# Kernel optimization log

Measured on AMD Instinct MI355X. Metric: run time of the kernel, lower is better.

## Reference

```python
import jax, jax.numpy as jnp
import numpy as np

N = 30000      # points
E = 400000     # edges
CIN = 16       # input point features
B = 4          # graphs in batch
H, W = 60, 80  # BEV grid


def _mlp_params(key, cin, cout):
    k1, k2 = jax.random.split(key)
    wa = jax.random.normal(k1, (cin, cout), jnp.float32) * np.float32(np.sqrt(2.0 / cin))
    wb = jax.random.normal(k2, (cout, cout), jnp.float32) * np.float32(np.sqrt(2.0 / cout))
    return wa, jnp.zeros((cout,), jnp.float32), wb, jnp.zeros((cout,), jnp.float32)


def setup_inputs() -> dict:
    key = jax.random.key(0)
    ks = jax.random.split(key, 8)
    x = jax.random.normal(ks[0], (N, CIN), jnp.float32)
    r = jax.random.uniform(ks[1], (N, 3), jnp.float32)
    Z = 1.0 + 9.0 * r[:, 2]
    X = (r[:, 0] - 0.5) * 1.2 * Z   # |X/Z| < 0.6 -> mostly inside image
    Y = (r[:, 1] - 0.5) * 0.9 * Z
    pos = jnp.stack([X, Y, Z], axis=1)
    edge_index = jax.random.randint(ks[2], (2, E), 0, N, jnp.int32)
    batch = jnp.sort(jax.random.randint(ks[3], (N,), 0, B, jnp.int32))
    K = jnp.array([[500.0, 0.0, 320.0], [0.0, 500.0, 240.0], [0.0, 0.0, 1.0]], jnp.float32)
    w11, b11, w12, b12 = _mlp_params(ks[4], CIN + 3, 64)
    w21, b21, w22, b22 = _mlp_params(ks[5], 64 + 3, 128)
    w31, b31, w32, b32 = _mlp_params(ks[6], 128 + 3, 256)
    return dict(x=x, pos=pos, K=K,
                w11=w11, b11=b11, w12=w12, b12=b12,
                w21=w21, b21=b21, w22=w22, b22=b22,
                w31=w31, b31=b31, w32=w32, b32=b32,
                edge_index=edge_index, batch=batch)


def _mlp(h, wa, ba, wb, bb):
    return jax.nn.relu(h @ wa + ba) @ wb + bb


def _pointnet_conv(feat, rel, src, dst, wa, ba, wb, bb):
    # PyG PointNetConv: msg = local_nn([x_j, pos_j - pos_i]); max-aggregate at target i
    msg = _mlp(jnp.concatenate([feat[src], rel], axis=1), wa, ba, wb, bb)
    agg = jax.ops.segment_max(msg, dst, num_segments=N)
    return jnp.where(jnp.isfinite(agg), agg, 0.0)  # empty segments -> 0 (PyG fill)


def _points_to_image(feat, pos, batch, K):
    X, Y, Z = pos[:, 0], pos[:, 1], pos[:, 2]
    u = ((K[0, 0] * X / Z + K[0, 2]) / 640.0 * W).astype(jnp.int32)  # trunc like .long()
    v = ((K[1, 1] * Y / Z + K[1, 2]) / 480.0 * H).astype(jnp.int32)
    mask = (u >= 0) & (u < W) & (v >= 0) & (v < H)
    idx = jnp.where(mask, batch * (H * W) + v * W + u, 0)
    contrib = feat * mask[:, None].astype(feat.dtype)
    flat = jnp.zeros((B * H * W, feat.shape[1]), feat.dtype).at[idx].add(contrib)
    return flat.reshape(B, H, W, feat.shape[1]).transpose(0, 3, 1, 2)


def reference(x, pos, K, w11, b11, w12, b12, w21, b21, w22, b22, w31, b31, w32, b32,
              edge_index, batch):
    src, dst = edge_index[0], edge_index[1]
    rel = pos[src] - pos[dst]
    h = _pointnet_conv(x, rel, src, dst, w11, b11, w12, b12)
    h = _pointnet_conv(h, rel, src, dst, w21, b21, w22, b22)
    h = _pointnet_conv(h, rel, src, dst, w31, b31, w32, b32)
    return _points_to_image(h, pos, batch, K)  # [B, 256, H, W]
```

## Files before the change

kernel.cpp:

```cpp
#include <hip/hip_runtime.h>
#include <math.h>

#define NN 30000
#define NE 400000

typedef _Float16 f16;
typedef _Float16 f16x8 __attribute__((ext_vector_type(8)));
typedef float f32x4 __attribute__((ext_vector_type(4)));

__device__ __forceinline__ void atomic_max_f(float* addr, float v) {
    if (v >= 0.0f) {
        atomicMax((int*)addr, __float_as_int(v));
    } else {
        atomicMin((unsigned int*)addr, __float_as_uint(v));
    }
}

__global__ __launch_bounds__(256) void fill_neg_inf(float* p, int n) {
    int i = blockIdx.x * blockDim.x + threadIdx.x;
    int stride = gridDim.x * blockDim.x;
    for (; i < n; i += stride) p[i] = -INFINITY;
}

__global__ __launch_bounds__(256) void hist_dst(const int* __restrict__ dst,
                                                int* __restrict__ counts) {
    int e = blockIdx.x * 256 + threadIdx.x;
    if (e < NE) atomicAdd(&counts[dst[e]], 1);
}

__global__ __launch_bounds__(1024) void scan_counts(const int* __restrict__ counts,
                                                    int* __restrict__ cursor) {
    __shared__ int lsum[1024];
    const int t = threadIdx.x;
    const int base = t * 30;
    int s = 0;
    for (int i = 0; i < 30; ++i) {
        int idx = base + i;
        if (idx < NN) s += counts[idx];
    }
    lsum[t] = s;
    __syncthreads();
    int acc = s;
    for (int off = 1; off < 1024; off <<= 1) {
        int v = (t >= off) ? lsum[t - off] : 0;
        __syncthreads();
        acc += v;
        lsum[t] = acc;
        __syncthreads();
    }
    int run = acc - s;
    for (int i = 0; i < 30; ++i) {
        int idx = base + i;
        if (idx < NN) { cursor[idx] = run; run += counts[idx]; }
    }
}

__global__ __launch_bounds__(256) void scatter_edges(const int* __restrict__ src,
                                                     const int* __restrict__ dst,
                                                     int* __restrict__ cursor,
                                                     int* __restrict__ srcS,
                                                     int* __restrict__ dstS) {
    int e = blockIdx.x * 256 + threadIdx.x;
    if (e >= NE) return;
    int d = dst[e];
    int p = atomicAdd(&cursor[d], 1);
    srcS[p] = src[e];
    dstS[p] = d;
}

template<int K, int N>
__global__ __launch_bounds__(256) void pack_w(const float* __restrict__ wsrc,
                                              f16* __restrict__ pB) {
    int f = blockIdx.x * 256 + threadIdx.x;
    if (f >= K * N) return;
    int j = f & 7;
    int l = (f >> 3) & 63;
    int rest = f >> 9;
    constexpr int KS = K / 32;
    int ks = rest % KS;
    int nt = rest / KS;
    int k = ks * 32 + ((l >> 4) << 3) + j;
    int n = nt * 16 + (l & 15);
    pB[f] = (f16)wsrc[k * N + n];
}

template<int K, int COUT>
__global__ __launch_bounds__(256) void node_linear(const float* __restrict__ feat,
                                                   const float* __restrict__ wa,
                                                   const float* __restrict__ b,
                                                   f16* __restrict__ A) {
    constexpr int NPB = 8;
    constexpr int G   = 256 / COUT;
    constexpr int NPT = NPB / G;
    __shared__ float sf[NPB * K];
    const int node0 = blockIdx.x * NPB;
    for (int idx = threadIdx.x; idx < NPB * K; idx += 256) {
        float v = feat[node0 * K + idx];
        if (!isfinite(v)) v = 0.0f;
        sf[idx] = v;
    }
    __syncthreads();
    const int j  = threadIdx.x % COUT;
    const int g  = threadIdx.x / COUT;
    const int n0 = g * NPT;
    float acc[NPT];
#pragma unroll
    for (int i = 0; i < NPT; i++) acc[i] = 0.0f;
    for (int k = 0; k < K; k++) {
        float w = wa[k * COUT + j];
#pragma unroll
        for (int nn = 0; nn < NPT; nn++)
            acc[nn] = fmaf(sf[(n0 + nn) * K + k], w, acc[nn]);
    }
    const float bj = b[j];
#pragma unroll
    for (int nn = 0; nn < NPT; nn++)
        A[(size_t)(node0 + n0 + nn) * COUT + j] = (f16)(acc[nn] + bj);
}

template<int K, int C>
__global__ __launch_bounds__(256) void node_gemm(const float* __restrict__ feat,
                                                 const f16* __restrict__ pW,
                                                 const float* __restrict__ bias,
                                                 f16* __restrict__ A) {
    constexpr int NTW = C / 64;
    constexpr int KS  = K / 32;
    __shared__ __align__(16) unsigned char smem[64 * K * 2];
    const int tid = threadIdx.x;
    const int node0 = blockIdx.x * 64;

    {
        const int e = tid >> 2, p = tid & 3;
        const bool valid = (node0 + e) < NN;
        const float* frow = feat + (size_t)(node0 + e) * K;
#pragma unroll
        for (int ch = 0; ch < K / 32; ++ch) {
            const int j0 = (ch * 4 + p) * 8;
            f16x8 hv;
#pragma unroll
            for (int jj = 0; jj < 8; ++jj) {
                float v = valid ? frow[j0 + jj] : 0.0f;
                if (!isfinite(v)) v = 0.0f;
                hv[jj] = (f16)v;
            }
            *(f16x8*)(smem + e * (K * 2) + ((j0 * 2) ^ ((e & 7) << 4))) = hv;
        }
    }
    __syncthreads();

    const int w = tid >> 6, l = tid & 63, lr = l & 15, lg = l >> 4;
    f32x4 acc[4][NTW];
#pragma unroll
    for (int m = 0; m < 4; ++m)
#pragma unroll
        for (int nt = 0; nt < NTW; ++nt) {
            acc[m][nt][0] = 0.f; acc[m][nt][1] = 0.f;
            acc[m][nt][2] = 0.f; acc[m][nt][3] = 0.f;
        }
#pragma unroll
    for (int ks = 0; ks < KS; ++ks) {
        f16x8 af[4];
#pragma unroll
        for (int m = 0; m < 4; ++m) {
            const int row = m * 16 + lr;
            af[m] = *(const f16x8*)(smem + row * (K * 2)
                     + (((ks * 32 + lg * 8) * 2) ^ ((row & 7) << 4)));
        }
#pragma unroll
        for (int nt = 0; nt < NTW; ++nt) {
            const int ntg = w * NTW + nt;
            f16x8 bf = *(const f16x8*)(pW + ((size_t)(ntg * KS + ks) * 64 + l) * 8);
#pragma unroll
            for (int m = 0; m < 4; ++m)
                acc[m][nt] = __builtin_amdgcn_mfma_f32_16x16x32_f16(af[m], bf, acc[m][nt], 0, 0, 0);
        }
    }
#pragma unroll
    for (int m = 0; m < 4; ++m)
#pragma unroll
        for (int nt = 0; nt < NTW; ++nt) {
            const int col = w * (C / 4) + nt * 16 + lr;
            const float bv = bias[col];
#pragma unroll
            for (int rr = 0; rr < 4; ++rr) {
                const int row = m * 16 + lg * 4 + rr;
                if (node0 + row < NN)
                    A[(size_t)(node0 + row) * C + col] = (f16)(acc[m][nt][rr] + bv);
            }
        }
}

template<int C>
__global__ __launch_bounds__(256) void edge_mfma(const f16* __restrict__ Ah,
                                                 const float* __restrict__ warel,
                                                 const f16* __restrict__ pB,
                                                 const float* __restrict__ bb,
                                                 const float* __restrict__ pos,
                                                 const int* __restrict__ srcS,
                                                 const int* __restrict__ dstS,
                                                 float* __restrict__ agg) {
    constexpr int TE  = 64;
    constexpr int NTW = C / 64;
    constexpr int KS  = C / 32;
    __shared__ __align__(16) unsigned char smem[TE * C * 2];
    __shared__ float s_warel[3 * C];
    __shared__ float s_rx[TE], s_ry[TE], s_rz[TE];
    __shared__ int s_src[TE], s_dst[TE];

    const int tid = threadIdx.x;
    const int nwg = gridDim.x;
    const int q = nwg >> 3, r = nwg & 7;
    const int xcd = blockIdx.x & 7, o = blockIdx.x >> 3;
    const int bid = (xcd < r ? xcd * (q + 1) : r * (q + 1) + (xcd - r) * q) + o;
    const int e0 = bid * TE;

    if (tid < TE) {
        int s = srcS[e0 + tid], d = dstS[e0 + tid];
        s_src[tid] = s; s_dst[tid] = d;
        s_rx[tid] = pos[3 * s + 0] - pos[3 * d + 0];
        s_ry[tid] = pos[3 * s + 1] - pos[3 * d + 1];
        s_rz[tid] = pos[3 * s + 2] - pos[3 * d + 2];
    }
    for (int i = tid; i < 3 * C; i += 256) s_warel[i] = warel[i];
    __syncthreads();

    {
        const int e = tid >> 2, p = tid & 3;
        const int s = s_src[e];
        const float rx = s_rx[e], ry = s_ry[e], rz = s_rz[e];
        const f16* arow = Ah + (size_t)s * C;
#pragma unroll
        for (int ch = 0; ch < C / 32; ++ch) {
            const int j0 = (ch * 4 + p) * 8;
            f16x8 av = *(const f16x8*)(arow + j0);
            f16x8 hv;
#pragma unroll
            for (int jj = 0; jj < 8; ++jj) {
                int jc = j0 + jj;
                float v = (float)av[jj] + rx * s_warel[jc] + ry * s_warel[C + jc]
                        + rz * s_warel[2 * C + jc];
                hv[jj] = (f16)fmaxf(v, 0.0f);
            }
            *(f16x8*)(smem + e * (C * 2) + ((j0 * 2) ^ ((e & 7) << 4))) = hv;
        }
    }
    __syncthreads();

    const int w = tid >> 6, l = tid & 63, lr = l & 15, lg = l >> 4;
    f32x4 acc[4][NTW];
#pragma unroll
    for (int m = 0; m < 4; ++m)
#pragma unroll
        for (int nt = 0; nt < NTW; ++nt) {
            acc[m][nt][0] = 0.f; acc[m][nt][1] = 0.f;
            acc[m][nt][2] = 0.f; acc[m][nt][3] = 0.f;
        }
#pragma unroll
    for (int ks = 0; ks < KS; ++ks) {
        f16x8 af[4];
#pragma unroll
        for (int m = 0; m < 4; ++m) {
            const int row = m * 16 + lr;
            af[m] = *(const f16x8*)(smem + row * (C * 2)
                     + (((ks * 32 + lg * 8) * 2) ^ ((row & 7) << 4)));
        }
#pragma unroll
        for (int nt = 0; nt < NTW; ++nt) {
            const int ntg = w * NTW + nt;
            f16x8 bf = *(const f16x8*)(pB + ((size_t)(ntg * KS + ks) * 64 + l) * 8);
#pragma unroll
            for (int m = 0; m < 4; ++m)
                acc[m][nt] = __builtin_amdgcn_mfma_f32_16x16x32_f16(af[m], bf, acc[m][nt], 0, 0, 0);
        }
    }

    float* msg = (float*)smem;
    const int c = tid;
    const bool active = (c < C);
    const float bbv = active ? bb[c] : 0.0f;
    float run = -INFINITY;
    int prev = s_dst[0];
#pragma unroll
    for (int half = 0; half < 2; ++half) {
        __syncthreads();
#pragma unroll
        for (int mi = 0; mi < 2; ++mi) {
            const int m = half * 2 + mi;
#pragma unroll
            for (int nt = 0; nt < NTW; ++nt) {
                const int col = w * (C / 4) + nt * 16 + lr;
#pragma unroll
                for (int rr = 0; rr < 4; ++rr) {
                    const int row = m * 16 + lg * 4 + rr;
                    msg[(row - half * 32) * C + col] = acc[m][nt][rr];
                }
            }
        }
        __syncthreads();
        if (active) {
            for (int e2 = 0; e2 < 32; ++e2) {
                const int d = s_dst[half * 32 + e2];
                const float v = msg[e2 * C + c];
                if (d != prev) {
                    atomic_max_f(&agg[(size_t)prev * C + c], run + bbv);
                    run = v; prev = d;
                } else {
                    run = fmaxf(run, v);
                }
            }
        }
    }
    if (active) atomic_max_f(&agg[(size_t)prev * C + c], run + bbv);
}

__global__ __launch_bounds__(256) void scatter_img(const float* __restrict__ feat,
                                                   const float* __restrict__ pos,
                                                   const float* __restrict__ Km,
                                                   const int* __restrict__ batch,
                                                   float* __restrict__ img) {
    const int n = blockIdx.x;
    const float X = pos[3 * n + 0], Y = pos[3 * n + 1], Z = pos[3 * n + 2];
    const float k00 = Km[0], k02 = Km[2], k11 = Km[4], k12 = Km[5];
    const int u = (int)((k00 * X / Z + k02) / 640.0f * 80.0f);
    const int v = (int)((k11 * Y / Z + k12) / 480.0f * 60.0f);
    if (u < 0 || u >= 80 || v < 0 || v >= 60) return;
    const int p = (batch[n] * 60 + v) * 80 + u;
    const int c = threadIdx.x;
    float val = feat[(size_t)n * 256 + c];
    if (!isfinite(val)) val = 0.0f;
    atomicAdd(img + (size_t)p * 256 + c, val);
}

__global__ __launch_bounds__(256) void transpose_img(const float* __restrict__ img,
                                                     float* __restrict__ out) {
    __shared__ float tile[32][33];
    const int b = blockIdx.z;
    const int p0 = blockIdx.x * 32, c0 = blockIdx.y * 32;
    const float* src = img + (size_t)b * 4800 * 256;
    float* dst = out + (size_t)b * 256 * 4800;
    const int tx = threadIdx.x & 31, ty = threadIdx.x >> 5;
#pragma unroll
    for (int i = 0; i < 32; i += 8)
        tile[ty + i][tx] = src[(size_t)(p0 + ty + i) * 256 + c0 + tx];
    __syncthreads();
#pragma unroll
    for (int i = 0; i < 32; i += 8)
        dst[(size_t)(c0 + ty + i) * 4800 + p0 + tx] = tile[tx][ty + i];
}

extern "C" void kernel_launch(void* const* d_in, const int* in_sizes, int n_in,
                              void* d_out, int out_size, void* d_ws, size_t ws_size,
                              hipStream_t stream) {
    const float* x   = (const float*)d_in[0];
    const float* pos = (const float*)d_in[1];
    const float* Km  = (const float*)d_in[2];
    const float* w11 = (const float*)d_in[3];
    const float* b11 = (const float*)d_in[4];
    const float* w12 = (const float*)d_in[5];
    const float* b12 = (const float*)d_in[6];
    const float* w21 = (const float*)d_in[7];
    const float* b21 = (const float*)d_in[8];
    const float* w22 = (const float*)d_in[9];
    const float* b22 = (const float*)d_in[10];
    const float* w31 = (const float*)d_in[11];
    const float* b31 = (const float*)d_in[12];
    const float* w32 = (const float*)d_in[13];
    const float* b32 = (const float*)d_in[14];
    const int* edge  = (const int*)d_in[15];
    const int* batch = (const int*)d_in[16];
    const int* srcp = edge;
    const int* dstp = edge + NE;
    float* out = (float*)d_out;

    float* aggA  = (float*)d_ws;
    float* aggB  = aggA + (size_t)NN * 256;
    f16*   Ah    = (f16*)(aggB + (size_t)NN * 256);
    int*   srcS  = (int*)(Ah + (size_t)NN * 256);
    int*   dstS  = srcS + NE;
    int*   counts = dstS + NE;
    int*   cursor = counts + NN;
    f16*   pW1   = (f16*)(cursor + NN);
    f16*   pW2   = pW1 + 64 * 64;
    f16*   pW3   = pW2 + 128 * 128;
    f16*   pW2n  = pW3 + 256 * 256;
    f16*   pW3n  = pW2n + 64 * 128;

    hipMemsetAsync(counts, 0, NN * sizeof(int), stream);
    hist_dst<<<(NE + 255) / 256, 256, 0, stream>>>(dstp, counts);
    scan_counts<<<1, 1024, 0, stream>>>(counts, cursor);
    scatter_edges<<<(NE + 255) / 256, 256, 0, stream>>>(srcp, dstp, cursor, srcS, dstS);

    pack_w<64, 64><<<(64 * 64 + 255) / 256, 256, 0, stream>>>(w12, pW1);
    pack_w<128, 128><<<(128 * 128 + 255) / 256, 256, 0, stream>>>(w22, pW2);
    pack_w<256, 256><<<(256 * 256 + 255) / 256, 256, 0, stream>>>(w32, pW3);
    pack_w<64, 128><<<(64 * 128 + 255) / 256, 256, 0, stream>>>(w21, pW2n);
    pack_w<128, 256><<<(128 * 256 + 255) / 256, 256, 0, stream>>>(w31, pW3n);

    node_linear<16, 64><<<NN / 8, 256, 0, stream>>>(x, w11, b11, Ah);
    fill_neg_inf<<<512, 256, 0, stream>>>(aggB, NN * 64);
    edge_mfma<64><<<NE / 64, 256, 0, stream>>>(Ah, w11 + 16 * 64, pW1, b12,
                                               pos, srcS, dstS, aggB);
    node_gemm<64, 128><<<(NN + 63) / 64, 256, 0, stream>>>(aggB, pW2n, b21, Ah);
    fill_neg_inf<<<512, 256, 0, stream>>>(aggA, NN * 128);
    edge_mfma<128><<<NE / 64, 256, 0, stream>>>(Ah, w21 + 64 * 128, pW2, b22,
                                                pos, srcS, dstS, aggA);
    node_gemm<128, 256><<<(NN + 63) / 64, 256, 0, stream>>>(aggA, pW3n, b31, Ah);
    fill_neg_inf<<<512, 256, 0, stream>>>(aggB, NN * 256);
    edge_mfma<256><<<NE / 64, 256, 0, stream>>>(Ah, w31 + 128 * 256, pW3, b32,
                                                pos, srcS, dstS, aggB);
    hipMemsetAsync(aggA, 0, (size_t)4 * 4800 * 256 * sizeof(float), stream);
    scatter_img<<<NN, 256, 0, stream>>>(aggB, pos, Km, batch, aggA);
    transpose_img<<<dim3(150, 8, 4), 256, 0, stream>>>(aggA, out);
}
```

Baseline: 423.7 us.

## Reduce segment max directly from MFMA registers and vectorize f16 first layer

```diff
diff --git a/kernel.cpp b/kernel.cpp
--- a/kernel.cpp
+++ b/kernel.cpp
@@ -84,6 +84,12 @@
     pB[f] = (f16)wsrc[k * N + n];
 }
 
+__global__ __launch_bounds__(256) void cast_f16(const float* __restrict__ w,
+                                                f16* __restrict__ o, int n) {
+    int i = blockIdx.x * 256 + threadIdx.x;
+    if (i < n) o[i] = (f16)w[i];
+}
+
 template<int K, int COUT>
 __global__ __launch_bounds__(256) void node_linear(const float* __restrict__ feat,
                                                    const float* __restrict__ wa,
@@ -149,14 +155,7 @@
     __syncthreads();
 
     const int w = tid >> 6, l = tid & 63, lr = l & 15, lg = l >> 4;
-    f32x4 acc[4][NTW];
-#pragma unroll
-    for (int m = 0; m < 4; ++m)
-#pragma unroll
-        for (int nt = 0; nt < NTW; ++nt) {
-            acc[m][nt][0] = 0.f; acc[m][nt][1] = 0.f;
-            acc[m][nt][2] = 0.f; acc[m][nt][3] = 0.f;
-        }
+    f32x4 acc[4][NTW] = {};
 #pragma unroll
     for (int ks = 0; ks < KS; ++ks) {
         f16x8 af[4];
@@ -192,7 +191,7 @@
 
 template<int C>
 __global__ __launch_bounds__(256) void edge_mfma(const f16* __restrict__ Ah,
-                                                 const float* __restrict__ warel,
+                                                 const f16* __restrict__ warelh,
                                                  const f16* __restrict__ pB,
                                                  const float* __restrict__ bb,
                                                  const float* __restrict__ pos,
@@ -202,8 +201,7 @@
     constexpr int TE  = 64;
     constexpr int NTW = C / 64;
     constexpr int KS  = C / 32;
-    __shared__ __align__(16) unsigned char smem[TE * C * 2];
-    __shared__ float s_warel[3 * C];
+    __shared__ __align__(16) unsigned char h1[TE * C * 2];
     __shared__ float s_rx[TE], s_ry[TE], s_rz[TE];
     __shared__ int s_src[TE], s_dst[TE];
 
@@ -221,96 +219,94 @@
         s_ry[tid] = pos[3 * s + 1] - pos[3 * d + 1];
         s_rz[tid] = pos[3 * s + 2] - pos[3 * d + 2];
     }
-    for (int i = tid; i < 3 * C; i += 256) s_warel[i] = warel[i];
     __syncthreads();
 
     {
         const int e = tid >> 2, p = tid & 3;
         const int s = s_src[e];
-        const float rx = s_rx[e], ry = s_ry[e], rz = s_rz[e];
+        const f16 rx = (f16)s_rx[e], ry = (f16)s_ry[e], rz = (f16)s_rz[e];
+        const f16x8 rxv = {rx, rx, rx, rx, rx, rx, rx, rx};
+        const f16x8 ryv = {ry, ry, ry, ry, ry, ry, ry, ry};
+        const f16x8 rzv = {rz, rz, rz, rz, rz, rz, rz, rz};
         const f16* arow = Ah + (size_t)s * C;
 #pragma unroll
         for (int ch = 0; ch < C / 32; ++ch) {
             const int j0 = (ch * 4 + p) * 8;
             f16x8 av = *(const f16x8*)(arow + j0);
-            f16x8 hv;
-#pragma unroll
-            for (int jj = 0; jj < 8; ++jj) {
-                int jc = j0 + jj;
-                float v = (float)av[jj] + rx * s_warel[jc] + ry * s_warel[C + jc]
-                        + rz * s_warel[2 * C + jc];
-                hv[jj] = (f16)fmaxf(v, 0.0f);
-            }
-            *(f16x8*)(smem + e * (C * 2) + ((j0 * 2) ^ ((e & 7) << 4))) = hv;
+            f16x8 w0 = *(const f16x8*)(warelh + j0);
+            f16x8 w1 = *(const f16x8*)(warelh + C + j0);
+            f16x8 w2 = *(const f16x8*)(warelh + 2 * C + j0);
+            f16x8 hv = av + rxv * w0 + ryv * w1 + rzv * w2;
+#pragma unroll
+            for (int jj = 0; jj < 8; ++jj)
+                hv[jj] = hv[jj] > (f16)0.f ? hv[jj] : (f16)0.f;
+            *(f16x8*)(h1 + e * (C * 2) + ((j0 * 2) ^ ((e & 7) << 4))) = hv;
         }
     }
     __syncthreads();
 
     const int w = tid >> 6, l = tid & 63, lr = l & 15, lg = l >> 4;
-    f32x4 acc[4][NTW];
-#pragma unroll
-    for (int m = 0; m < 4; ++m)
-#pragma unroll
-        for (int nt = 0; nt < NTW; ++nt) {
-            acc[m][nt][0] = 0.f; acc[m][nt][1] = 0.f;
-            acc[m][nt][2] = 0.f; acc[m][nt][3] = 0.f;
-        }
+    f32x4 acc[4][NTW] = {};
+    f16x8 bfc[NTW], bfn[NTW];
+#pragma unroll
+    for (int nt = 0; nt < NTW; ++nt)
+        bfc[nt] = *(const f16x8*)(pB + ((size_t)((w * NTW + nt) * KS) * 64 + l) * 8);
 #pragma unroll
     for (int ks = 0; ks < KS; ++ks) {
+        if (ks + 1 < KS) {
+#pragma unroll
+            for (int nt = 0; nt < NTW; ++nt)
+                bfn[nt] = *(const f16x8*)(pB + ((size_t)((w * NTW + nt) * KS + ks + 1) * 64 + l) * 8);
+        }
         f16x8 af[4];
 #pragma unroll
         for (int m = 0; m < 4; ++m) {
             const int row = m * 16 + lr;
-            af[m] = *(const f16x8*)(smem + row * (C * 2)
+            af[m] = *(const f16x8*)(h1 + row * (C * 2)
                      + (((ks * 32 + lg * 8) * 2) ^ ((row & 7) << 4)));
         }
 #pragma unroll
+        for (int nt = 0; nt < NTW; ++nt)
+#pragma unroll
+            for (int m = 0; m < 4; ++m)
+                acc[m][nt] = __builtin_amdgcn_mfma_f32_16x16x32_f16(af[m], bfc[nt], acc[m][nt], 0, 0, 0);
+#pragma unroll
+        for (int nt = 0; nt < NTW; ++nt) bfc[nt] = bfn[nt];
+    }
+
+    float bbv[NTW];
+#pragma unroll
+    for (int nt = 0; nt < NTW; ++nt) bbv[nt] = bb[w * (C / 4) + nt * 16 + lr];
+
+    const int myd = s_dst[l];
+    const int pd  = s_dst[l == 0 ? 0 : l - 1];
+    unsigned long long m = __ballot((l == 0) || (myd != pd));
+
+    while (m) {
+        const int a = __builtin_ctzll(m);
+        const unsigned long long m2 = m & (m - 1);
+        const int b = m2 ? __builtin_ctzll(m2) : 64;
+        m = m2;
+        const int d = s_dst[a];
+#pragma unroll
         for (int nt = 0; nt < NTW; ++nt) {
-            const int ntg = w * NTW + nt;
-            f16x8 bf = *(const f16x8*)(pB + ((size_t)(ntg * KS + ks) * 64 + l) * 8);
-#pragma unroll
-            for (int m = 0; m < 4; ++m)
-                acc[m][nt] = __builtin_amdgcn_mfma_f32_16x16x32_f16(af[m], bf, acc[m][nt], 0, 0, 0);
-        }
-    }
-
-    float* msg = (float*)smem;
-    const int c = tid;
-    const bool active = (c < C);
-    const float bbv = active ? bb[c] : 0.0f;
-    float run = -INFINITY;
-    int prev = s_dst[0];
-#pragma unroll
-    for (int half = 0; half < 2; ++half) {
-        __syncthreads();
-#pragma unroll
-        for (int mi = 0; mi < 2; ++mi) {
-            const int m = half * 2 + mi;
-#pragma unroll
-            for (int nt = 0; nt < NTW; ++nt) {
-                const int col = w * (C / 4) + nt * 16 + lr;
+            float v = -INFINITY;
+#pragma unroll
+            for (int mm = 0; mm < 4; ++mm) {
+                if (b <= mm * 16 || a >= mm * 16 + 16) continue;
 #pragma unroll
                 for (int rr = 0; rr < 4; ++rr) {
-                    const int row = m * 16 + lg * 4 + rr;
-                    msg[(row - half * 32) * C + col] = acc[m][nt][rr];
+                    const int row = mm * 16 + lg * 4 + rr;
+                    const bool in = (row >= a) && (row < b);
+                    v = fmaxf(v, in ? acc[mm][nt][rr] : -INFINITY);
                 }
             }
-        }
-        __syncthreads();
-        if (active) {
-            for (int e2 = 0; e2 < 32; ++e2) {
-                const int d = s_dst[half * 32 + e2];
-                const float v = msg[e2 * C + c];
-                if (d != prev) {
-                    atomic_max_f(&agg[(size_t)prev * C + c], run + bbv);
-                    run = v; prev = d;
-                } else {
-                    run = fmaxf(run, v);
-                }
-            }
-        }
-    }
-    if (active) atomic_max_f(&agg[(size_t)prev * C + c], run + bbv);
+            v = fmaxf(v, __shfl_xor(v, 16, 64));
+            v = fmaxf(v, __shfl_xor(v, 32, 64));
+            if (lg == 0)
+                atomic_max_f(&agg[(size_t)d * C + w * (C / 4) + nt * 16 + lr], v + bbv[nt]);
+        }
+    }
 }
 
 __global__ __launch_bounds__(256) void scatter_img(const float* __restrict__ feat,
@@ -384,6 +380,9 @@
     f16*   pW3   = pW2 + 128 * 128;
     f16*   pW2n  = pW3 + 256 * 256;
     f16*   pW3n  = pW2n + 64 * 128;
+    f16*   wr1   = pW3n + 128 * 256;
+    f16*   wr2   = wr1 + 3 * 64;
+    f16*   wr3   = wr2 + 3 * 128;
 
     hipMemsetAsync(counts, 0, NN * sizeof(int), stream);
     hist_dst<<<(NE + 255) / 256, 256, 0, stream>>>(dstp, counts);
@@ -395,18 +394,21 @@
     pack_w<256, 256><<<(256 * 256 + 255) / 256, 256, 0, stream>>>(w32, pW3);
     pack_w<64, 128><<<(64 * 128 + 255) / 256, 256, 0, stream>>>(w21, pW2n);
     pack_w<128, 256><<<(128 * 256 + 255) / 256, 256, 0, stream>>>(w31, pW3n);
+    cast_f16<<<1, 256, 0, stream>>>(w11 + 16 * 64, wr1, 3 * 64);
+    cast_f16<<<2, 256, 0, stream>>>(w21 + 64 * 128, wr2, 3 * 128);
+    cast_f16<<<3, 256, 0, stream>>>(w31 + 128 * 256, wr3, 3 * 256);
 
     node_linear<16, 64><<<NN / 8, 256, 0, stream>>>(x, w11, b11, Ah);
     fill_neg_inf<<<512, 256, 0, stream>>>(aggB, NN * 64);
-    edge_mfma<64><<<NE / 64, 256, 0, stream>>>(Ah, w11 + 16 * 64, pW1, b12,
+    edge_mfma<64><<<NE / 64, 256, 0, stream>>>(Ah, wr1, pW1, b12,
                                                pos, srcS, dstS, aggB);
     node_gemm<64, 128><<<(NN + 63) / 64, 256, 0, stream>>>(aggB, pW2n, b21, Ah);
     fill_neg_inf<<<512, 256, 0, stream>>>(aggA, NN * 128);
-    edge_mfma<128><<<NE / 64, 256, 0, stream>>>(Ah, w21 + 64 * 128, pW2, b22,
+    edge_mfma<128><<<NE / 64, 256, 0, stream>>>(Ah, wr2, pW2, b22,
                                                 pos, srcS, dstS, aggA);
     node_gemm<128, 256><<<(NN + 63) / 64, 256, 0, stream>>>(aggA, pW3n, b31, Ah);
     fill_neg_inf<<<512, 256, 0, stream>>>(aggB, NN * 256);
-    edge_mfma<256><<<NE / 64, 256, 0, stream>>>(Ah, w31 + 128 * 256, pW3, b32,
+    edge_mfma<256><<<NE / 64, 256, 0, stream>>>(Ah, wr3, pW3, b32,
                                                 pos, srcS, dstS, aggB);
     hipMemsetAsync(aggA, 0, (size_t)4 * 4800 * 256 * sizeof(float), stream);
     scatter_img<<<NN, 256, 0, stream>>>(aggB, pos, Km, batch, aggA);
```

Result: slower. 440.5 us (+4.0%).
